# Kernel optimization log

Measured on AMD Instinct MI355X. Metric: run time of the kernel, lower is better.

## Reference

```python
import jax, jax.numpy as jnp
import numpy as np

BSZ = 2048
L = 64            # sequence length, power of 2
D = 15            # symbol_repr_size
NC = 10           # n_classes; embedding row NC is the 'inf' token
TREE_LEN = 2 * L - 1  # next_power_of_2(L)*2 - 1


def rms_norm(x):
    # x / (sqrt(mean(x^2, -1) + 1e-6) + 1e-6)
    return x / (jnp.sqrt(jnp.mean(x * x, axis=-1, keepdims=True) + 1e-6) + 1e-6)


def setup_inputs() -> dict:
    key = jax.random.key(0)
    k1, k2, k3, k4, k5 = jax.random.split(key, 5)
    x = jax.random.randint(k1, (BSZ, L), 0, NC)
    q = jnp.sort(jax.random.randint(k2, (BSZ, 2), 0, L), axis=1)  # low <= high
    query_low, query_high = q[:, 0], q[:, 1]
    emb = jax.random.normal(k3, (NC + 1, D), dtype=jnp.float32)
    W_lin = jax.random.normal(k4, (NC, D), dtype=jnp.float32) * 0.26   # ~1/sqrt(D)
    W_rule = jax.random.normal(k5, (2, D * D), dtype=jnp.float32) * 0.066  # ~1/D
    return {"emb": emb, "W_lin": W_lin, "W_rule": W_rule,
            "x": x, "query_low": query_low, "query_high": query_high}


def reference(emb, W_lin, W_rule, x, query_low, query_high):
    def combine(a, b):
        # outer product [b, D, D] -> rule linear (225 -> 2) -> softmax mix
        inp = jnp.einsum('bi,bj->bij', a, b).reshape(a.shape[0], -1)
        alpha = jax.nn.softmax(inp @ W_rule.T, axis=-1)  # [b, 2]
        return alpha[:, :1] * a + alpha[:, 1:] * b

    def build(trees, lst, low, high, pos):
        # recursive segment-tree build; low/high/pos are static Python ints
        if low == high:
            return rms_norm(trees.at[:, pos, :].set(lst[:, low, :]))
        mid = (low + high) // 2
        trees = build(trees, lst, low, mid, 2 * pos + 1)
        trees = build(trees, lst, mid + 1, high, 2 * pos + 2)
        mix = combine(trees[:, 2 * pos + 1], trees[:, 2 * pos + 2])
        return rms_norm(trees.at[:, pos, :].set(mix))

    inf_raw = emb[NC]  # raw inf token used inside query (no rms_norm in torch)

    def query(trees, returns, low, high, pos):
        if pos >= TREE_LEN:
            return returns
        f = returns.dtype
        mA = ((query_low <= low) & (query_high >= high)).astype(f)[:, None]
        returns = mA * trees[:, pos] + (1 - mA) * returns
        mB = ((query_low > high) | (query_high < low)).astype(f)[:, None]
        returns = mB * inf_raw[None, :] + (1 - mB) * returns
        mC = (1 - mA) * (1 - mB)
        mid = (low + high) // 2
        a1 = query(trees, returns, low, mid, 2 * pos + 1)
        a2 = query(trees, returns, mid + 1, high, 2 * pos + 2)
        new = combine(a1, a2)
        return rms_norm(mC * new + (1 - mC) * returns)

    h = rms_norm(emb[x])                              # [BSZ, L, D]
    inf_n = rms_norm(emb[NC][None, None, :])          # normalized inf token
    trees = jnp.broadcast_to(inf_n, (BSZ, TREE_LEN, D)) + jnp.zeros((), emb.dtype)
    trees = build(trees, h, 0, L - 1, 0)              # [BSZ, TREE_LEN, D]
    returns = jnp.zeros((BSZ, D), dtype=emb.dtype)
    returns = query(trees, returns, 0, L - 1, 0)      # [BSZ, D]
    return returns @ W_lin.T                          # [BSZ, NC]
```

## Files before the change

### kernel.cpp

```cpp
#include <hip/hip_runtime.h>
#include <math.h>

#define DD 15
#define DP 20
#define LL 64
#define NCC 10
#define NTREE 63
#define EPB 4

__device__ __forceinline__ float dpp_xor1(float x) {
    return __int_as_float(__builtin_amdgcn_update_dpp(0, __float_as_int(x), 0xB1, 0xF, 0xF, true));
}
__device__ __forceinline__ float dpp_xor2(float x) {
    return __int_as_float(__builtin_amdgcn_update_dpp(0, __float_as_int(x), 0x4E, 0xF, 0xF, true));
}
__device__ __forceinline__ float dpp_hmirror(float x) {
    return __int_as_float(__builtin_amdgcn_update_dpp(0, __float_as_int(x), 0x141, 0xF, 0xF, true));
}

__device__ __forceinline__ void combine8_core(const float* Lrow, const float* Rrow,
                                              const float w[4][DD], int k, int qr, int u,
                                              float& o0, float& o1)
{
    float4 R0 = ((const float4*)Rrow)[0];
    float4 R1 = ((const float4*)Rrow)[1];
    float4 R2 = ((const float4*)Rrow)[2];
    float4 R3 = ((const float4*)Rrow)[3];
    float4 Aq = ((const float4*)Lrow)[qr];
    float Bv[DD] = {R0.x,R0.y,R0.z,R0.w, R1.x,R1.y,R1.z,R1.w,
                    R2.x,R2.y,R2.z,R2.w, R3.x,R3.y,R3.z};
    float Av[4] = {Aq.x, Aq.y, Aq.z, Aq.w};

    float p = 0.f;
    #pragma unroll
    for (int ri = 0; ri < 4; ++ri) {
        float d0 = 0.f;
        #pragma unroll
        for (int j = 0; j < DD; ++j) d0 = fmaf(w[ri][j], Bv[j], d0);
        p = fmaf(Av[ri], d0, p);
    }
    float a    = p + dpp_xor2(p);
    float hma  = dpp_hmirror(a);
    float self = a + dpp_xor1(hma);
    float oth  = dpp_xor1(a) + hma;
    float mx = fmaxf(self, oth);
    float es = __expf(self - mx), eo = __expf(oth - mx);
    float rs = __builtin_amdgcn_rcpf(es + eo);
    float aS = es * rs, aO = eo * rs;
    float a0 = (k == 0) ? aS : aO;
    float a1 = (k == 0) ? aO : aS;

    float2 lm = ((const float2*)Lrow)[u];
    float2 rm = ((const float2*)Rrow)[u];
    float v0 = a0 * lm.x + a1 * rm.x;
    float v1 = a0 * lm.y + a1 * rm.y;
    float ss = v0 * v0 + v1 * v1;
    ss += dpp_xor1(ss);
    ss += dpp_xor2(ss);
    ss += dpp_hmirror(ss);
    float inv = __builtin_amdgcn_rsqf(ss * (1.0f / DD) + 1e-6f);
    o0 = v0 * inv; o1 = v1 * inv;
}

__device__ __forceinline__ void build_level5(float (*tw)[DP], const float (*nemb)[DP],
                                             const float w[4][DD],
                                             const int xA[4], const int xB[4],
                                             int k, int qr, int u, int g)
{
    #pragma unroll
    for (int st = 0; st < 4; ++st) {
        int pi = st * 8 + g;
        float o0, o1;
        combine8_core(&nemb[xA[st]][0], &nemb[xB[st]][0], w, k, qr, u, o0, o1);
        ((float2*)&tw[31 + pi][0])[u] = make_float2(o0, o1);
    }
}

__device__ __forceinline__ void query_level5(float (*tw)[DP], const float (*nemb)[DP],
                                             const float w[4][DD], int t, int k, int qr, int u,
                                             int ql, int qh, int xq1, int xq2)
{
    const int g2 = (t >> 3) & 1;
    int bnd = g2 ? qh : ql;
    int piB = bnd >> 1;
    int lo = 2 * piB, hi = lo + 1;
    bool full = (ql <= lo) && (qh >= hi);
    bool d1 = (ql > lo) || (qh < lo);
    bool d2 = (ql > hi) || (qh < hi);
    const float* Lrow = d1 ? &nemb[NCC][0] : &nemb[xq1][0];
    const float* Rrow = d2 ? &nemb[NCC][0] : &nemb[xq2][0];
    float o0, o1;
    combine8_core(Lrow, Rrow, w, k, qr, u, o0, o1);
    bool we = (!full) && (t < 16) && (g2 == 0 || piB != (ql >> 1));
    if (we) ((float2*)&tw[31 + piB][0])[u] = make_float2(o0, o1);
}

template<int LVL>
__device__ __forceinline__ void build_level(float (*tw)[DP], const float w[4][DD],
                                            int k, int qr, int u, int g)
{
    constexpr int n = 1 << LVL, first = n - 1, nst = (n + 7) / 8;
    #pragma unroll
    for (int st = 0; st < nst; ++st) {
        int pi0 = st * 8 + g;
        int pi = (n < 8) ? ((pi0 < n) ? pi0 : 0) : pi0;
        int p = first + pi;
        float o0, o1;
        combine8_core(&tw[2 * p + 1][0], &tw[2 * p + 2][0], w, k, qr, u, o0, o1);
        if (pi0 < n)
            ((float2*)&tw[p][0])[u] = make_float2(o0, o1);
    }
}

template<int LVL>
__device__ __forceinline__ void query_level(float (*tw)[DP], const float (*nemb)[DP],
                                            const float w[4][DD], int t, int k, int qr, int u,
                                            int ql, int qh)
{
    constexpr int first = (1 << LVL) - 1;
    constexpr int sh = 6 - LVL;
    constexpr int shc = sh - 1;
    const int g2 = (t >> 3) & 1;
    int bnd = g2 ? qh : ql;
    int pi = bnd >> sh;
    int lo = pi << sh, hi = lo + (1 << sh) - 1;
    bool full = (ql <= lo) && (qh >= hi);
    int p = first + pi;
    int ci1 = 2 * pi, ci2 = 2 * pi + 1;
    int lo1 = ci1 << shc, hi1 = lo1 + (1 << shc) - 1;
    int lo2 = ci2 << shc, hi2 = lo2 + (1 << shc) - 1;
    bool d1 = (ql > hi1) || (qh < lo1);
    bool d2 = (ql > hi2) || (qh < lo2);
    const float* Lrow = d1 ? &nemb[NCC][0] : &tw[2 * p + 1][0];
    const float* Rrow = d2 ? &nemb[NCC][0] : &tw[2 * p + 2][0];
    float o0, o1;
    combine8_core(Lrow, Rrow, w, k, qr, u, o0, o1);
    bool we = (!full) && (t < 16) && (g2 == 0 || pi != (ql >> sh));
    if (we) ((float2*)&tw[p][0])[u] = make_float2(o0, o1);
}

__device__ __forceinline__ void query_level0(float (*tw)[DP], const float (*nemb)[DP],
                                             const float w[4][DD], int t, int k, int qr, int u,
                                             int ql, int qh)
{
    bool d1 = (ql > 31);
    bool d2 = (qh < 32);
    const float* Lrow = d1 ? &nemb[NCC][0] : &tw[1][0];
    const float* Rrow = d2 ? &nemb[NCC][0] : &tw[2][0];
    float o0, o1;
    combine8_core(Lrow, Rrow, w, k, qr, u, o0, o1);
    if (t < 8) ((float2*)&tw[0][0])[u] = make_float2(o0, o1);
}

extern "C" __global__ __attribute__((amdgpu_flat_work_group_size(256, 256)))
void seg_tree_kernel(
    const float* __restrict__ emb,
    const float* __restrict__ W_lin,
    const float* __restrict__ W_rule,
    const int*  __restrict__ x,
    const int*  __restrict__ qlo_g,
    const int*  __restrict__ qhi_g,
    float* __restrict__ out,
    int bsz)
{
    __shared__ __align__(16) float nemb[NCC + 1][DP];
    __shared__ __align__(16) float tree[EPB][NTREE][DP];

    const int tb = threadIdx.x;
    const int wv = tb >> 6;
    const int t  = tb & 63;
    int b = blockIdx.x * EPB + wv;
    const bool active = (b < bsz);
    if (!active) b = bsz - 1;

    const int k = t & 1, qr = (t >> 1) & 3, u = t & 7, g = t >> 3;
    float (*tw)[DP] = tree[wv];

    const int ql = qlo_g[b], qh = qhi_g[b];
    int xA[4], xB[4];
    #pragma unroll
    for (int st = 0; st < 4; ++st) {
        xA[st] = x[b * LL + st * 16 + 2 * g];
        xB[st] = x[b * LL + st * 16 + 2 * g + 1];
    }
    int piB = (((t >> 3) & 1) ? qh : ql) >> 1;
    int xq1 = x[b * LL + 2 * piB], xq2 = x[b * LL + 2 * piB + 1];

    float w[4][DD];
    #pragma unroll
    for (int ri = 0; ri < 4; ++ri) {
        int i = 4 * qr + ri;
        bool valid = (i < DD);
        const float* src = W_rule + k * DD * DD + (valid ? i * DD : 0);
        #pragma unroll
        for (int j = 0; j < DD; ++j) w[ri][j] = valid ? src[j] : 0.0f;
    }
    #pragma unroll
    for (int ri = 0; ri < 4; ++ri)
        #pragma unroll
        for (int j = 0; j < DD; ++j)
            asm("" : "+v"(w[ri][j]));

    if (tb < NCC + 1) {
        float v[DD]; float ssum = 0.f;
        #pragma unroll
        for (int d = 0; d < DD; ++d) { v[d] = emb[tb * DD + d]; ssum += v[d] * v[d]; }
        float inv = __builtin_amdgcn_rsqf(ssum * (1.0f / DD) + 1e-6f);
        #pragma unroll
        for (int d = 0; d < DD; ++d) nemb[tb][d] = v[d] * inv;
        nemb[tb][DD] = 0.0f;
    }
    __syncthreads();

    build_level5(tw, nemb, w, xA, xB, k, qr, u, g);
    query_level5(tw, nemb, w, t, k, qr, u, ql, qh, xq1, xq2);

    build_level<4>(tw, w, k, qr, u, g);
    query_level<4>(tw, nemb, w, t, k, qr, u, ql, qh);

    build_level<3>(tw, w, k, qr, u, g);
    query_level<3>(tw, nemb, w, t, k, qr, u, ql, qh);

    build_level<2>(tw, w, k, qr, u, g);
    query_level<2>(tw, nemb, w, t, k, qr, u, ql, qh);

    build_level<1>(tw, w, k, qr, u, g);
    query_level<1>(tw, nemb, w, t, k, qr, u, ql, qh);

    query_level0(tw, nemb, w, t, k, qr, u, ql, qh);

    if (active && t < NCC) {
        float acc = 0.f;
        #pragma unroll
        for (int d = 0; d < DD; ++d) acc = fmaf(tw[0][d], W_lin[t * DD + d], acc);
        out[b * NCC + t] = acc;
    }
}

extern "C" void kernel_launch(void* const* d_in, const int* in_sizes, int n_in,
                              void* d_out, int out_size, void* d_ws, size_t ws_size,
                              hipStream_t stream) {
    const float* emb    = (const float*)d_in[0];
    const float* W_lin  = (const float*)d_in[1];
    const float* W_rule = (const float*)d_in[2];
    const int*   x      = (const int*)d_in[3];
    const int*   qlo    = (const int*)d_in[4];
    const int*   qhi    = (const int*)d_in[5];
    float* outp = (float*)d_out;

    int bsz = in_sizes[3] / LL;
    int nblk = (bsz + EPB - 1) / EPB;
    seg_tree_kernel<<<dim3(nblk), dim3(256), 0, stream>>>(
        emb, W_lin, W_rule, x, qlo, qhi, outp, bsz);
}
```

Before: 15.33 us.

## Build only segment-tree nodes fully inside the query range

```diff
diff --git a/kernel.cpp b/kernel.cpp
--- a/kernel.cpp
+++ b/kernel.cpp
@@ -34,10 +34,12 @@
     float p = 0.f;
     #pragma unroll
     for (int ri = 0; ri < 4; ++ri) {
-        float d0 = 0.f;
-        #pragma unroll
-        for (int j = 0; j < DD; ++j) d0 = fmaf(w[ri][j], Bv[j], d0);
-        p = fmaf(Av[ri], d0, p);
+        float dA = 0.f, dB = 0.f;
+        #pragma unroll
+        for (int j = 0; j < 8; ++j)  dA = fmaf(w[ri][j], Bv[j], dA);
+        #pragma unroll
+        for (int j = 8; j < DD; ++j) dB = fmaf(w[ri][j], Bv[j], dB);
+        p = fmaf(Av[ri], dA + dB, p);
     }
     float a    = p + dpp_xor2(p);
     float hma  = dpp_hmirror(a);
@@ -60,20 +62,6 @@
     ss += dpp_hmirror(ss);
     float inv = __builtin_amdgcn_rsqf(ss * (1.0f / DD) + 1e-6f);
     o0 = v0 * inv; o1 = v1 * inv;
-}
-
-__device__ __forceinline__ void build_level5(float (*tw)[DP], const float (*nemb)[DP],
-                                             const float w[4][DD],
-                                             const int xA[4], const int xB[4],
-                                             int k, int qr, int u, int g)
-{
-    #pragma unroll
-    for (int st = 0; st < 4; ++st) {
-        int pi = st * 8 + g;
-        float o0, o1;
-        combine8_core(&nemb[xA[st]][0], &nemb[xB[st]][0], w, k, qr, u, o0, o1);
-        ((float2*)&tw[31 + pi][0])[u] = make_float2(o0, o1);
-    }
 }
 
 __device__ __forceinline__ void query_level5(float (*tw)[DP], const float (*nemb)[DP],
@@ -93,23 +81,6 @@
     combine8_core(Lrow, Rrow, w, k, qr, u, o0, o1);
     bool we = (!full) && (t < 16) && (g2 == 0 || piB != (ql >> 1));
     if (we) ((float2*)&tw[31 + piB][0])[u] = make_float2(o0, o1);
-}
-
-template<int LVL>
-__device__ __forceinline__ void build_level(float (*tw)[DP], const float w[4][DD],
-                                            int k, int qr, int u, int g)
-{
-    constexpr int n = 1 << LVL, first = n - 1, nst = (n + 7) / 8;
-    #pragma unroll
-    for (int st = 0; st < nst; ++st) {
-        int pi0 = st * 8 + g;
-        int pi = (n < 8) ? ((pi0 < n) ? pi0 : 0) : pi0;
-        int p = first + pi;
-        float o0, o1;
-        combine8_core(&tw[2 * p + 1][0], &tw[2 * p + 2][0], w, k, qr, u, o0, o1);
-        if (pi0 < n)
-            ((float2*)&tw[p][0])[u] = make_float2(o0, o1);
-    }
 }
 
 template<int LVL>
@@ -176,7 +147,15 @@
     const int k = t & 1, qr = (t >> 1) & 3, u = t & 7, g = t >> 3;
     float (*tw)[DP] = tree[wv];
 
-    const int ql = qlo_g[b], qh = qhi_g[b];
+    const int ql = __builtin_amdgcn_readfirstlane(qlo_g[b]);
+    const int qh = __builtin_amdgcn_readfirstlane(qhi_g[b]);
+
+    const int plo5 = (ql + 1) >> 1, phi5 = (qh + 1) >> 1;
+    const int plo4 = (ql + 3) >> 2, phi4 = (qh + 1) >> 2;
+    const int plo3 = (ql + 7) >> 3, phi3 = (qh + 1) >> 3;
+    const int plo2 = (ql + 15) >> 4, phi2 = (qh + 1) >> 4;
+    const int plo1 = (ql + 31) >> 5, phi1 = (qh + 1) >> 5;
+
     int xA[4], xB[4];
     #pragma unroll
     for (int st = 0; st < 4; ++st) {
@@ -212,19 +191,54 @@
     }
     __syncthreads();
 
-    build_level5(tw, nemb, w, xA, xB, k, qr, u, g);
+    {
+        int st_lo = plo5 >> 3, st_hi = (phi5 + 7) >> 3;
+        for (int st = st_lo; st < st_hi; ++st) {
+            int pi0 = st * 8 + g;
+            float o0, o1;
+            combine8_core(&nemb[xA[st]][0], &nemb[xB[st]][0], w, k, qr, u, o0, o1);
+            if (pi0 >= plo5 && pi0 < phi5)
+                ((float2*)&tw[31 + pi0][0])[u] = make_float2(o0, o1);
+        }
+    }
     query_level5(tw, nemb, w, t, k, qr, u, ql, qh, xq1, xq2);
 
-    build_level<4>(tw, w, k, qr, u, g);
+    {
+        int st_lo = plo4 >> 3, st_hi = (phi4 + 7) >> 3;
+        for (int st = st_lo; st < st_hi; ++st) {
+            int pi0 = st * 8 + g;
+            float o0, o1;
+            combine8_core(&tw[31 + 2 * pi0][0], &tw[32 + 2 * pi0][0], w, k, qr, u, o0, o1);
+            if (pi0 >= plo4 && pi0 < phi4)
+                ((float2*)&tw[15 + pi0][0])[u] = make_float2(o0, o1);
+        }
+    }
     query_level<4>(tw, nemb, w, t, k, qr, u, ql, qh);
 
-    build_level<3>(tw, w, k, qr, u, g);
+    if (phi3 > plo3) {
+        float o0, o1;
+        combine8_core(&tw[15 + 2 * g][0], &tw[16 + 2 * g][0], w, k, qr, u, o0, o1);
+        if (g >= plo3 && g < phi3)
+            ((float2*)&tw[7 + g][0])[u] = make_float2(o0, o1);
+    }
     query_level<3>(tw, nemb, w, t, k, qr, u, ql, qh);
 
-    build_level<2>(tw, w, k, qr, u, g);
+    if (phi2 > plo2) {
+        int pi = g & 3;
+        float o0, o1;
+        combine8_core(&tw[7 + 2 * pi][0], &tw[8 + 2 * pi][0], w, k, qr, u, o0, o1);
+        if (g < 4 && pi >= plo2 && pi < phi2)
+            ((float2*)&tw[3 + pi][0])[u] = make_float2(o0, o1);
+    }
     query_level<2>(tw, nemb, w, t, k, qr, u, ql, qh);
 
-    build_level<1>(tw, w, k, qr, u, g);
+    if (phi1 > plo1) {
+        int pi = g & 1;
+        float o0, o1;
+        combine8_core(&tw[3 + 2 * pi][0], &tw[4 + 2 * pi][0], w, k, qr, u, o0, o1);
+        if (g < 2 && pi >= plo1 && pi < phi1)
+            ((float2*)&tw[1 + pi][0])[u] = make_float2(o0, o1);
+    }
     query_level<1>(tw, nemb, w, t, k, qr, u, ql, qh);
 
     query_level0(tw, nemb, w, t, k, qr, u, ql, qh);
```

Measured after the change: 16.28 us. +6.2%, slower.

## Batch LDS child loads per level before compute, simplify softmax, preload W_lin

Applied to the files above, without the earlier changes.

```diff
diff --git a/kernel.cpp b/kernel.cpp
--- a/kernel.cpp
+++ b/kernel.cpp
@@ -18,42 +18,52 @@
     return __int_as_float(__builtin_amdgcn_update_dpp(0, __float_as_int(x), 0x141, 0xF, 0xF, true));
 }
 
-__device__ __forceinline__ void combine8_core(const float* Lrow, const float* Rrow,
-                                              const float w[4][DD], int k, int qr, int u,
-                                              float& o0, float& o1)
+struct CR {
+    float4 Lq;
+    float4 R0, R1, R2, R3;
+    float2 lm, rm;
+};
+
+__device__ __forceinline__ CR load_children(const float* Lrow, const float* Rrow, int qr, int u) {
+    CR c;
+    c.Lq = ((const float4*)Lrow)[qr];
+    c.R0 = ((const float4*)Rrow)[0];
+    c.R1 = ((const float4*)Rrow)[1];
+    c.R2 = ((const float4*)Rrow)[2];
+    c.R3 = ((const float4*)Rrow)[3];
+    c.lm = ((const float2*)Lrow)[u];
+    c.rm = ((const float2*)Rrow)[u];
+    return c;
+}
+
+__device__ __forceinline__ void compute_combine(const CR& c, const float w[4][DD], int k,
+                                                float& o0, float& o1)
 {
-    float4 R0 = ((const float4*)Rrow)[0];
-    float4 R1 = ((const float4*)Rrow)[1];
-    float4 R2 = ((const float4*)Rrow)[2];
-    float4 R3 = ((const float4*)Rrow)[3];
-    float4 Aq = ((const float4*)Lrow)[qr];
-    float Bv[DD] = {R0.x,R0.y,R0.z,R0.w, R1.x,R1.y,R1.z,R1.w,
-                    R2.x,R2.y,R2.z,R2.w, R3.x,R3.y,R3.z};
-    float Av[4] = {Aq.x, Aq.y, Aq.z, Aq.w};
+    float Bv[DD] = {c.R0.x,c.R0.y,c.R0.z,c.R0.w, c.R1.x,c.R1.y,c.R1.z,c.R1.w,
+                    c.R2.x,c.R2.y,c.R2.z,c.R2.w, c.R3.x,c.R3.y,c.R3.z};
+    float Av[4] = {c.Lq.x, c.Lq.y, c.Lq.z, c.Lq.w};
 
     float p = 0.f;
     #pragma unroll
     for (int ri = 0; ri < 4; ++ri) {
-        float d0 = 0.f;
-        #pragma unroll
-        for (int j = 0; j < DD; ++j) d0 = fmaf(w[ri][j], Bv[j], d0);
-        p = fmaf(Av[ri], d0, p);
+        float dA = 0.f, dB = 0.f;
+        #pragma unroll
+        for (int j = 0; j < 8; ++j)  dA = fmaf(w[ri][j], Bv[j], dA);
+        #pragma unroll
+        for (int j = 8; j < DD; ++j) dB = fmaf(w[ri][j], Bv[j], dB);
+        p = fmaf(Av[ri], dA + dB, p);
     }
     float a    = p + dpp_xor2(p);
     float hma  = dpp_hmirror(a);
     float self = a + dpp_xor1(hma);
     float oth  = dpp_xor1(a) + hma;
-    float mx = fmaxf(self, oth);
-    float es = __expf(self - mx), eo = __expf(oth - mx);
-    float rs = __builtin_amdgcn_rcpf(es + eo);
-    float aS = es * rs, aO = eo * rs;
+    float aS = __builtin_amdgcn_rcpf(1.0f + __expf(oth - self));
+    float aO = 1.0f - aS;
     float a0 = (k == 0) ? aS : aO;
     float a1 = (k == 0) ? aO : aS;
 
-    float2 lm = ((const float2*)Lrow)[u];
-    float2 rm = ((const float2*)Rrow)[u];
-    float v0 = a0 * lm.x + a1 * rm.x;
-    float v1 = a0 * lm.y + a1 * rm.y;
+    float v0 = fmaf(a0, c.lm.x, a1 * c.rm.x);
+    float v1 = fmaf(a0, c.lm.y, a1 * c.rm.y);
     float ss = v0 * v0 + v1 * v1;
     ss += dpp_xor1(ss);
     ss += dpp_xor2(ss);
@@ -62,94 +72,50 @@
     o0 = v0 * inv; o1 = v1 * inv;
 }
 
-__device__ __forceinline__ void build_level5(float (*tw)[DP], const float (*nemb)[DP],
-                                             const float w[4][DD],
-                                             const int xA[4], const int xB[4],
-                                             int k, int qr, int u, int g)
+template<int LVL>
+__device__ __forceinline__ void phase(float (*tw)[DP], const float (*nemb)[DP],
+                                      const float w[4][DD], int t, int k, int qr, int u, int g,
+                                      int ql, int qh)
 {
-    #pragma unroll
-    for (int st = 0; st < 4; ++st) {
-        int pi = st * 8 + g;
-        float o0, o1;
-        combine8_core(&nemb[xA[st]][0], &nemb[xB[st]][0], w, k, qr, u, o0, o1);
-        ((float2*)&tw[31 + pi][0])[u] = make_float2(o0, o1);
-    }
-}
-
-__device__ __forceinline__ void query_level5(float (*tw)[DP], const float (*nemb)[DP],
-                                             const float w[4][DD], int t, int k, int qr, int u,
-                                             int ql, int qh, int xq1, int xq2)
-{
+    constexpr int n = 1 << LVL, first = n - 1;
+    constexpr int NB = (n > 8) ? (n / 8) : 1;
+    constexpr int sh = 6 - LVL, shc = sh - 1;
+
+    CR cb[NB]; int pb[NB];
+    #pragma unroll
+    for (int st = 0; st < NB; ++st) {
+        int pi = (n >= 8) ? (st * 8 + g) : (g & (n - 1));
+        int p = first + pi;
+        pb[st] = p;
+        cb[st] = load_children(&tw[2 * p + 1][0], &tw[2 * p + 2][0], qr, u);
+    }
     const int g2 = (t >> 3) & 1;
     int bnd = g2 ? qh : ql;
-    int piB = bnd >> 1;
-    int lo = 2 * piB, hi = lo + 1;
+    int piq = bnd >> sh;
+    int pq = first + piq;
+    int lo = piq << sh, hi = lo + (1 << sh) - 1;
     bool full = (ql <= lo) && (qh >= hi);
-    bool d1 = (ql > lo) || (qh < lo);
-    bool d2 = (ql > hi) || (qh < hi);
-    const float* Lrow = d1 ? &nemb[NCC][0] : &nemb[xq1][0];
-    const float* Rrow = d2 ? &nemb[NCC][0] : &nemb[xq2][0];
-    float o0, o1;
-    combine8_core(Lrow, Rrow, w, k, qr, u, o0, o1);
-    bool we = (!full) && (t < 16) && (g2 == 0 || piB != (ql >> 1));
-    if (we) ((float2*)&tw[31 + piB][0])[u] = make_float2(o0, o1);
-}
-
-template<int LVL>
-__device__ __forceinline__ void build_level(float (*tw)[DP], const float w[4][DD],
-                                            int k, int qr, int u, int g)
-{
-    constexpr int n = 1 << LVL, first = n - 1, nst = (n + 7) / 8;
-    #pragma unroll
-    for (int st = 0; st < nst; ++st) {
-        int pi0 = st * 8 + g;
-        int pi = (n < 8) ? ((pi0 < n) ? pi0 : 0) : pi0;
-        int p = first + pi;
-        float o0, o1;
-        combine8_core(&tw[2 * p + 1][0], &tw[2 * p + 2][0], w, k, qr, u, o0, o1);
-        if (pi0 < n)
-            ((float2*)&tw[p][0])[u] = make_float2(o0, o1);
-    }
-}
-
-template<int LVL>
-__device__ __forceinline__ void query_level(float (*tw)[DP], const float (*nemb)[DP],
-                                            const float w[4][DD], int t, int k, int qr, int u,
-                                            int ql, int qh)
-{
-    constexpr int first = (1 << LVL) - 1;
-    constexpr int sh = 6 - LVL;
-    constexpr int shc = sh - 1;
-    const int g2 = (t >> 3) & 1;
-    int bnd = g2 ? qh : ql;
-    int pi = bnd >> sh;
-    int lo = pi << sh, hi = lo + (1 << sh) - 1;
-    bool full = (ql <= lo) && (qh >= hi);
-    int p = first + pi;
-    int ci1 = 2 * pi, ci2 = 2 * pi + 1;
-    int lo1 = ci1 << shc, hi1 = lo1 + (1 << shc) - 1;
-    int lo2 = ci2 << shc, hi2 = lo2 + (1 << shc) - 1;
+    int lo1 = (2 * piq) << shc,     hi1 = lo1 + (1 << shc) - 1;
+    int lo2 = (2 * piq + 1) << shc, hi2 = lo2 + (1 << shc) - 1;
     bool d1 = (ql > hi1) || (qh < lo1);
     bool d2 = (ql > hi2) || (qh < lo2);
-    const float* Lrow = d1 ? &nemb[NCC][0] : &tw[2 * p + 1][0];
-    const float* Rrow = d2 ? &nemb[NCC][0] : &tw[2 * p + 2][0];
-    float o0, o1;
-    combine8_core(Lrow, Rrow, w, k, qr, u, o0, o1);
-    bool we = (!full) && (t < 16) && (g2 == 0 || pi != (ql >> sh));
-    if (we) ((float2*)&tw[p][0])[u] = make_float2(o0, o1);
-}
-
-__device__ __forceinline__ void query_level0(float (*tw)[DP], const float (*nemb)[DP],
-                                             const float w[4][DD], int t, int k, int qr, int u,
-                                             int ql, int qh)
-{
-    bool d1 = (ql > 31);
-    bool d2 = (qh < 32);
-    const float* Lrow = d1 ? &nemb[NCC][0] : &tw[1][0];
-    const float* Rrow = d2 ? &nemb[NCC][0] : &tw[2][0];
-    float o0, o1;
-    combine8_core(Lrow, Rrow, w, k, qr, u, o0, o1);
-    if (t < 8) ((float2*)&tw[0][0])[u] = make_float2(o0, o1);
+    const float* Lp = d1 ? &nemb[NCC][0] : &tw[2 * pq + 1][0];
+    const float* Rp = d2 ? &nemb[NCC][0] : &tw[2 * pq + 2][0];
+    CR cq = load_children(Lp, Rp, qr, u);
+
+    #pragma unroll
+    for (int st = 0; st < NB; ++st) {
+        float o0, o1;
+        compute_combine(cb[st], w, k, o0, o1);
+        if (n >= 8 || g < n)
+            ((float2*)&tw[pb[st]][0])[u] = make_float2(o0, o1);
+    }
+    {
+        float o0, o1;
+        compute_combine(cq, w, k, o0, o1);
+        bool we = (!full) && (t < 16) && (g2 == 0 || piq != (ql >> sh));
+        if (we) ((float2*)&tw[pq][0])[u] = make_float2(o0, o1);
+    }
 }
 
 extern "C" __global__ __attribute__((amdgpu_flat_work_group_size(256, 256)))
@@ -177,13 +143,15 @@
     float (*tw)[DP] = tree[wv];
 
     const int ql = qlo_g[b], qh = qhi_g[b];
+
     int xA[4], xB[4];
     #pragma unroll
     for (int st = 0; st < 4; ++st) {
         xA[st] = x[b * LL + st * 16 + 2 * g];
         xB[st] = x[b * LL + st * 16 + 2 * g + 1];
     }
-    int piB = (((t >> 3) & 1) ? qh : ql) >> 1;
+    const int g2i = (t >> 3) & 1;
+    int piB = (g2i ? qh : ql) >> 1;
     int xq1 = x[b * LL + 2 * piB], xq2 = x[b * LL + 2 * piB + 1];
 
     float w[4][DD];
@@ -201,6 +169,13 @@
         for (int j = 0; j < DD; ++j)
             asm("" : "+v"(w[ri][j]));
 
+    float wl[DD];
+    {
+        const float* wlp = W_lin + ((t < NCC) ? t : 0) * DD;
+        #pragma unroll
+        for (int d = 0; d < DD; ++d) wl[d] = wlp[d];
+    }
+
     if (tb < NCC + 1) {
         float v[DD]; float ssum = 0.f;
         #pragma unroll
@@ -212,27 +187,53 @@
     }
     __syncthreads();
 
-    build_level5(tw, nemb, w, xA, xB, k, qr, u, g);
-    query_level5(tw, nemb, w, t, k, qr, u, ql, qh, xq1, xq2);
-
-    build_level<4>(tw, w, k, qr, u, g);
-    query_level<4>(tw, nemb, w, t, k, qr, u, ql, qh);
-
-    build_level<3>(tw, w, k, qr, u, g);
-    query_level<3>(tw, nemb, w, t, k, qr, u, ql, qh);
-
-    build_level<2>(tw, w, k, qr, u, g);
-    query_level<2>(tw, nemb, w, t, k, qr, u, ql, qh);
-
-    build_level<1>(tw, w, k, qr, u, g);
-    query_level<1>(tw, nemb, w, t, k, qr, u, ql, qh);
-
-    query_level0(tw, nemb, w, t, k, qr, u, ql, qh);
+    {
+        CR c5[4];
+        #pragma unroll
+        for (int st = 0; st < 4; ++st)
+            c5[st] = load_children(&nemb[xA[st]][0], &nemb[xB[st]][0], qr, u);
+        int lo = 2 * piB, hi = lo + 1;
+        bool full5 = (ql <= lo) && (qh >= hi);
+        bool d1 = (ql > lo) || (qh < lo);
+        bool d2 = (ql > hi) || (qh < hi);
+        const float* Lp = d1 ? &nemb[NCC][0] : &nemb[xq1][0];
+        const float* Rp = d2 ? &nemb[NCC][0] : &nemb[xq2][0];
+        CR cq5 = load_children(Lp, Rp, qr, u);
+
+        #pragma unroll
+        for (int st = 0; st < 4; ++st) {
+            float o0, o1;
+            compute_combine(c5[st], w, k, o0, o1);
+            ((float2*)&tw[31 + st * 8 + g][0])[u] = make_float2(o0, o1);
+        }
+        {
+            float o0, o1;
+            compute_combine(cq5, w, k, o0, o1);
+            bool we = (!full5) && (t < 16) && (g2i == 0 || piB != (ql >> 1));
+            if (we) ((float2*)&tw[31 + piB][0])[u] = make_float2(o0, o1);
+        }
+    }
+
+    phase<4>(tw, nemb, w, t, k, qr, u, g, ql, qh);
+    phase<3>(tw, nemb, w, t, k, qr, u, g, ql, qh);
+    phase<2>(tw, nemb, w, t, k, qr, u, g, ql, qh);
+    phase<1>(tw, nemb, w, t, k, qr, u, g, ql, qh);
+
+    {
+        bool d1 = (ql > 31);
+        bool d2 = (qh < 32);
+        const float* Lp = d1 ? &nemb[NCC][0] : &tw[1][0];
+        const float* Rp = d2 ? &nemb[NCC][0] : &tw[2][0];
+        CR c0 = load_children(Lp, Rp, qr, u);
+        float o0, o1;
+        compute_combine(c0, w, k, o0, o1);
+        if (t < 8) ((float2*)&tw[0][0])[u] = make_float2(o0, o1);
+    }
 
     if (active && t < NCC) {
         float acc = 0.f;
         #pragma unroll
-        for (int d = 0; d < DD; ++d) acc = fmaf(tw[0][d], W_lin[t * DD + d], acc);
+        for (int d = 0; d < DD; ++d) acc = fmaf(tw[0][d], wl[d], acc);
         out[b * NCC + t] = acc;
     }
 }
```

New measurement: 15.50 us. About the same (+1.1%).
